# Performance work log

Measured on AMD Instinct MI355X. Metric: run time of the kernel, lower is better.

Reference implementation:

```python
import jax, jax.numpy as jnp
import numpy as np

N = 100000      # nodes (== hyperedges, H is square: adjacency-derived incidence)
NNZ = 3200000   # nonzeros in H
IN, HID, OUT = 512, 16, 64


def setup_inputs() -> dict:
    key = jax.random.key(0)
    ks = jax.random.split(key, 8)
    row = jax.random.randint(ks[0], (NNZ,), 0, N)
    col = jax.random.randint(ks[1], (NNZ,), 0, N)
    values = jnp.ones((NNZ,), dtype=jnp.float32)
    X = jax.random.normal(ks[2], (N, IN), dtype=jnp.float32)
    W1 = jax.random.normal(ks[3], (HID, IN), dtype=jnp.float32) * 0.05
    b1 = jax.random.normal(ks[4], (HID,), dtype=jnp.float32) * 0.05
    W2 = jax.random.normal(ks[5], (OUT, HID), dtype=jnp.float32) * 0.05
    b2 = jax.random.normal(ks[6], (OUT,), dtype=jnp.float32) * 0.05
    return {"row": row, "col": col, "values": values, "X": X,
            "W1": W1, "b1": b1, "W2": W2, "b2": b2}


def reference(row, col, values, X, W1, b1, W2, b2):
    # Degrees: d_V = H.sum(1) over rows, d_E = H.sum(0) over cols
    d_V = jax.ops.segment_sum(values, row, num_segments=N)
    d_E = jax.ops.segment_sum(values, col, num_segments=N)
    dv = d_V ** -0.5          # D_V^-1/2 diagonal
    de = d_E ** -1.0          # D_E^-1 diagonal (W = I, folded in)

    def conv(Y):
        # D_V^-1/2 @ H @ D_E^-1 @ H^T @ D_V^-1/2 @ Y, via edge-list SpMMs
        Y1 = Y * dv[:, None]
        # Z = H^T @ Y1 : scatter v * Y1[row] into hyperedge bins (col)
        Z = jax.ops.segment_sum(values[:, None] * Y1[row], col, num_segments=N)
        Z = Z * de[:, None]
        # O = H @ Z : scatter v * Z[col] back into node bins (row)
        O = jax.ops.segment_sum(values[:, None] * Z[col], row, num_segments=N)
        return O * dv[:, None]

    # dropout is identity in eval mode
    H1 = jax.nn.relu(conv(X @ W1.T + b1))      # [N, HID]
    out = conv(H1 @ W2.T + b2)                  # [N, OUT]
    return out
```

## Files before the change

### kernel.cpp

```cpp
#include <hip/hip_runtime.h>

#define NN 100000
#define NNZ 3200000
#define DIN 512
#define DHID 16
#define DOUT 64
#define NBUK 391
#define BCAP 9216
#define EPB 4096
#define NBLK_A ((NNZ + EPB - 1) / EPB)

#define GLOBAL_AS __attribute__((address_space(1)))
#define LDS_AS    __attribute__((address_space(3)))


__global__ __launch_bounds__(256) void init_cur_kernel(
    int* __restrict__ cur_c, int* __restrict__ cur_r) {
    int i = blockIdx.x * 256 + threadIdx.x;
    if (i < NBUK) { cur_c[i] = i * BCAP; cur_r[i] = i * BCAP; }
}

__global__ __launch_bounds__(256) void bucket_scatter_kernel(
    const int* __restrict__ row, const int* __restrict__ col,
    int* __restrict__ cur_c, int* __restrict__ cur_r,
    int* __restrict__ stgc, int* __restrict__ stgr) {
    __shared__ int stage[EPB];
    __shared__ unsigned short binOf[EPB];
    __shared__ int hist[512], scn[256], lof[512], curb[512], gdelta[512];
    int side = blockIdx.y;
    const int* key = side ? row : col;
    const int* oth = side ? col : row;
    int* gcur = side ? cur_r : cur_c;
    int* gstg = side ? stgr : stgc;
    int tid = threadIdx.x;
    int m = NNZ - blockIdx.x * EPB; if (m > EPB) m = EPB;
    int e0 = blockIdx.x * EPB + tid;

    hist[tid] = 0; hist[tid + 256] = 0;
    __syncthreads();
    #pragma unroll 4
    for (int u = 0; u < EPB / 256; ++u) {
        if (tid + u * 256 < m) atomicAdd(&hist[key[e0 + u * 256] >> 8], 1);
    }
    __syncthreads();
    int s0 = hist[2 * tid], s1 = hist[2 * tid + 1];
    int ps = s0 + s1;
    scn[tid] = ps;
    __syncthreads();
    for (int d = 1; d < 256; d <<= 1) {
        int t = (tid >= d) ? scn[tid - d] : 0;
        __syncthreads();
        scn[tid] += t;
        __syncthreads();
    }
    int excl = scn[tid] - ps;
    lof[2 * tid] = excl;
    lof[2 * tid + 1] = excl + s0;
    curb[2 * tid] = excl;
    curb[2 * tid + 1] = excl + s0;
    if (2 * tid < NBUK)
        gdelta[2 * tid] = (s0 ? atomicAdd(&gcur[2 * tid], s0) : (2 * tid) * BCAP) - excl;
    if (2 * tid + 1 < NBUK)
        gdelta[2 * tid + 1] = (s1 ? atomicAdd(&gcur[2 * tid + 1], s1) : (2 * tid + 1) * BCAP) - (excl + s0);
    __syncthreads();
    #pragma unroll 2
    for (int u = 0; u < EPB / 256; ++u) {
        if (tid + u * 256 < m) {
            int e = e0 + u * 256;
            int k = key[e], o2 = oth[e];
            int bin = k >> 8;
            int pos = atomicAdd(&curb[bin], 1);
            stage[pos] = ((k & 255) << 17) | o2;
            binOf[pos] = (unsigned short)bin;
        }
    }
    __syncthreads();
    for (int i = tid; i < m; i += 256) {
        int bin = binOf[i];
        int dst = gdelta[bin] + i;
        if (dst < (bin + 1) * BCAP) gstg[dst] = stage[i];
    }
}

__global__ __launch_bounds__(256) void bucket_finalize_kernel(
    const int* __restrict__ cur_c, const int* __restrict__ cur_r,
    const int* __restrict__ stgc, const int* __restrict__ stgr,
    int* __restrict__ adjc, int* __restrict__ adjr,
    int* __restrict__ os_c, int* __restrict__ oe_c,
    int* __restrict__ os_r, int* __restrict__ oe_r,
    float* __restrict__ dee, float* __restrict__ dvv) {
    int side = blockIdx.y;
    const int* curv = side ? cur_r : cur_c;
    const int* stg = side ? stgr : stgc;
    int* adj = side ? adjr : adjc;
    int* os = side ? os_r : os_c;
    int* oe = side ? oe_r : oe_c;
    __shared__ int E[BCAP];
    __shared__ int hist[256], cur[256], scn[256];
    int b = blockIdx.x, tid = threadIdx.x;
    int base = b * BCAP;
    int m = curv[b] - base;
    if (m > BCAP) m = BCAP;
    hist[tid] = 0;
    __syncthreads();
    for (int i = tid; i < m; i += 256) {
        int ev = stg[base + i];
        E[i] = ev;
        atomicAdd(&hist[ev >> 17], 1);
    }
    __syncthreads();
    int x = hist[tid];
    scn[tid] = x;
    __syncthreads();
    for (int d = 1; d < 256; d <<= 1) {
        int t = (tid >= d) ? scn[tid - d] : 0;
        __syncthreads();
        scn[tid] += t;
        __syncthreads();
    }
    int excl = scn[tid] - x;
    cur[tid] = excl;
    __syncthreads();
    for (int i = tid; i < m; i += 256) {
        int ev = E[i];
        int nl = ev >> 17;
        int pos = atomicAdd(&cur[nl], 1);
        adj[base + pos] = ev & 0x1FFFF;
    }
    int n = (b << 8) + tid;
    if (n < NN) {
        os[n] = base + excl;
        oe[n] = base + excl + x;
        float xf = (float)x;
        if (side == 0) dee[n] = x > 0 ? 1.0f / xf : 0.f;
        else           dvv[n] = x > 0 ? rsqrtf(xf) : 0.f;
    }
}

__global__ __launch_bounds__(256) void gemm1_kernel(
    const float* __restrict__ X, const float* __restrict__ W1,
    const float* __restrict__ b1, const float* __restrict__ dvv,
    float* __restrict__ Yv) {
    __shared__ float W1s[16 * 516];
    __shared__ float Xs0[16 * 260];
    __shared__ float Xs1[16 * 260];
    int tid = threadIdx.x;
    for (int it = 0; it < 8; ++it) {
        int idx = (it * 256 + tid) << 2;
        int h = idx >> 9, k = idx & 511;
        __builtin_amdgcn_global_load_lds(
            (const GLOBAL_AS void*)(W1 + idx),
            (LDS_AS void*)(W1s + h * 516 + k), 16, 0, 0);
    }
    int n0 = blockIdx.x << 4;
    for (int it = 0; it < 4; ++it) {
        int idx = (it * 256 + tid) << 2;
        int r = idx >> 8, k = idx & 255;
        __builtin_amdgcn_global_load_lds(
            (const GLOBAL_AS void*)(X + (size_t)(n0 + r) * DIN + k),
            (LDS_AS void*)(Xs0 + r * 260 + k), 16, 0, 0);
    }
    __syncthreads();
    for (int it = 0; it < 4; ++it) {
        int idx = (it * 256 + tid) << 2;
        int r = idx >> 8, k = idx & 255;
        __builtin_amdgcn_global_load_lds(
            (const GLOBAL_AS void*)(X + (size_t)(n0 + r) * DIN + 256 + k),
            (LDS_AS void*)(Xs1 + r * 260 + k), 16, 0, 0);
    }
    int n = tid >> 4, h = tid & 15;
    float4 a4 = make_float4(0.f, 0.f, 0.f, 0.f);
    {
        const float4* xr = reinterpret_cast<const float4*>(Xs0 + n * 260);
        const float4* wr = reinterpret_cast<const float4*>(W1s + h * 516);
        #pragma unroll 8
        for (int k4 = 0; k4 < 64; ++k4) {
            float4 xv = xr[k4], wv = wr[k4];
            a4.x = fmaf(xv.x, wv.x, a4.x);
            a4.y = fmaf(xv.y, wv.y, a4.y);
            a4.z = fmaf(xv.z, wv.z, a4.z);
            a4.w = fmaf(xv.w, wv.w, a4.w);
        }
    }
    __syncthreads();
    {
        const float4* xr = reinterpret_cast<const float4*>(Xs1 + n * 260);
        const float4* wr = reinterpret_cast<const float4*>(W1s + h * 516 + 256);
        #pragma unroll 8
        for (int k4 = 0; k4 < 64; ++k4) {
            float4 xv = xr[k4], wv = wr[k4];
            a4.x = fmaf(xv.x, wv.x, a4.x);
            a4.y = fmaf(xv.y, wv.y, a4.y);
            a4.z = fmaf(xv.z, wv.z, a4.z);
            a4.w = fmaf(xv.w, wv.w, a4.w);
        }
    }
    float acc = (a4.x + a4.y) + (a4.z + a4.w);
    int node = n0 + n;
    Yv[node * DHID + h] = (acc + b1[h]) * dvv[node];
}

template<int MODE, int FUSE1, int FUSEOUT>
__global__ __launch_bounds__(256) void gather16_kernel(
    const int* __restrict__ os, const int* __restrict__ oe,
    const int* __restrict__ adj, const float* __restrict__ src,
    const float* __restrict__ sc, const float* __restrict__ src1,
    const float* __restrict__ sc1, float* __restrict__ dst,
    float* __restrict__ dst1, const float* __restrict__ W2,
    const float* __restrict__ b2, const float* __restrict__ g1,
    float* __restrict__ outp) {
    __shared__ float W2t[16 * 64];
    __shared__ float b2s[64];
    int tid = threadIdx.x;
    if (FUSEOUT) {
        #pragma unroll
        for (int q = 0; q < 4; ++q) {
            int idx = (tid << 2) + q;
            int o = idx >> 4, h = idx & 15;
            W2t[h * 64 + o] = W2[idx];
        }
        if (tid < 64) b2s[tid] = b2[tid];
        __syncthreads();
    }
    int t = blockIdx.x * 256 + tid;
    int n = t >> 4, sub = (t >> 2) & 3, f4 = t & 3;
    const float4* src4 = reinterpret_cast<const float4*>(src);
    float4 a0 = make_float4(0.f, 0.f, 0.f, 0.f);
    float4 a1 = make_float4(0.f, 0.f, 0.f, 0.f);
    float4 a2 = make_float4(0.f, 0.f, 0.f, 0.f);
    float4 a3 = make_float4(0.f, 0.f, 0.f, 0.f);
    float acc1 = 0.f;
    int pe = oe[n];
    int p = os[n] + sub;
    for (; p + 12 < pe; p += 16) {
        int j0 = adj[p], j1 = adj[p + 4], j2 = adj[p + 8], j3 = adj[p + 12];
        float4 s0 = src4[(j0 << 2) | f4];
        float4 s1 = src4[(j1 << 2) | f4];
        float4 s2 = src4[(j2 << 2) | f4];
        float4 s3 = src4[(j3 << 2) | f4];
        a0.x += s0.x; a0.y += s0.y; a0.z += s0.z; a0.w += s0.w;
        a1.x += s1.x; a1.y += s1.y; a1.z += s1.z; a1.w += s1.w;
        a2.x += s2.x; a2.y += s2.y; a2.z += s2.z; a2.w += s2.w;
        a3.x += s3.x; a3.y += s3.y; a3.z += s3.z; a3.w += s3.w;
        if (FUSE1 && f4 == 0) acc1 += (src1[j0] + src1[j1]) + (src1[j2] + src1[j3]);
    }
    for (; p < pe; p += 4) {
        int j0 = adj[p];
        float4 s0 = src4[(j0 << 2) | f4];
        a0.x += s0.x; a0.y += s0.y; a0.z += s0.z; a0.w += s0.w;
        if (FUSE1 && f4 == 0) acc1 += src1[j0];
    }
    float4 acc;
    acc.x = (a0.x + a1.x) + (a2.x + a3.x);
    acc.y = (a0.y + a1.y) + (a2.y + a3.y);
    acc.z = (a0.z + a1.z) + (a2.z + a3.z);
    acc.w = (a0.w + a1.w) + (a2.w + a3.w);
    acc.x += __shfl_xor(acc.x, 4); acc.y += __shfl_xor(acc.y, 4);
    acc.z += __shfl_xor(acc.z, 4); acc.w += __shfl_xor(acc.w, 4);
    acc.x += __shfl_xor(acc.x, 8); acc.y += __shfl_xor(acc.y, 8);
    acc.z += __shfl_xor(acc.z, 8); acc.w += __shfl_xor(acc.w, 8);
    if (FUSE1 && f4 == 0) {
        acc1 += __shfl_xor(acc1, 4);
        acc1 += __shfl_xor(acc1, 8);
    }
    if (FUSEOUT) {
        float s = sc[n];
        float T[16];
        #pragma unroll
        for (int q = 0; q < 4; ++q) {
            T[4 * q + 0] = s * __shfl(acc.x, q, 16);
            T[4 * q + 1] = s * __shfl(acc.y, q, 16);
            T[4 * q + 2] = s * __shfl(acc.z, q, 16);
            T[4 * q + 3] = s * __shfl(acc.w, q, 16);
        }
        int l = tid & 15;
        float gn = g1[n];
        float4 o4 = make_float4(0.f, 0.f, 0.f, 0.f);
        #pragma unroll
        for (int h = 0; h < DHID; ++h) {
            float4 w = *reinterpret_cast<const float4*>(&W2t[h * 64 + 4 * l]);
            o4.x = fmaf(T[h], w.x, o4.x);
            o4.y = fmaf(T[h], w.y, o4.y);
            o4.z = fmaf(T[h], w.z, o4.z);
            o4.w = fmaf(T[h], w.w, o4.w);
        }
        float4 bb = *reinterpret_cast<const float4*>(&b2s[4 * l]);
        o4.x = fmaf(gn, bb.x, o4.x);
        o4.y = fmaf(gn, bb.y, o4.y);
        o4.z = fmaf(gn, bb.z, o4.z);
        o4.w = fmaf(gn, bb.w, o4.w);
        reinterpret_cast<float4*>(outp)[(n << 4) | l] = o4;
    } else if (sub == 0) {
        float s = sc[n];
        if (MODE == 1) {
            acc.x *= s; acc.y *= s; acc.z *= s; acc.w *= s;
        } else {
            acc.x = s * fmaxf(s * acc.x, 0.f);
            acc.y = s * fmaxf(s * acc.y, 0.f);
            acc.z = s * fmaxf(s * acc.z, 0.f);
            acc.w = s * fmaxf(s * acc.w, 0.f);
        }
        reinterpret_cast<float4*>(dst)[(n << 2) | f4] = acc;
        if (FUSE1 && f4 == 0) dst1[n] = acc1 * sc1[n];
    }
}

extern "C" void kernel_launch(void* const* d_in, const int* in_sizes, int n_in,
                              void* d_out, int out_size, void* d_ws, size_t ws_size,
                              hipStream_t stream) {
    const int*   row    = (const int*)d_in[0];
    const int*   col    = (const int*)d_in[1];
    const float* X      = (const float*)d_in[3];
    const float* W1     = (const float*)d_in[4];
    const float* b1     = (const float*)d_in[5];
    const float* W2     = (const float*)d_in[6];
    const float* b2     = (const float*)d_in[7];
    float* out = (float*)d_out;

    char* ws = (char*)d_ws;
    size_t o = 0;
    auto alloc = [&](size_t elems) {
        void* p = ws + o; o += (elems * 4 + 15) & ~size_t(15); return p;
    };

    int*   cur_c = (int*)alloc(NBUK);
    int*   cur_r = (int*)alloc(NBUK);
    int*   os_c  = (int*)alloc(NN);
    int*   oe_c  = (int*)alloc(NN);
    int*   os_r  = (int*)alloc(NN);
    int*   oe_r  = (int*)alloc(NN);
    float* dvv   = (float*)alloc(NN);
    float* dee   = (float*)alloc(NN);
    float* ue    = (float*)alloc(NN);
    float* gv    = (float*)alloc(NN);
    int*   stgc  = (int*)alloc((size_t)NBUK * BCAP);
    int*   stgr  = (int*)alloc((size_t)NBUK * BCAP);
    int*   adjc  = (int*)alloc((size_t)NBUK * BCAP);
    int*   adjr  = (int*)alloc((size_t)NBUK * BCAP);
    float* Yv    = (float*)alloc((size_t)NN * DHID);
    float* Z1    = (float*)alloc((size_t)NN * DHID);
    float* Sv    = (float*)alloc((size_t)NN * DHID);
    float* Z2    = (float*)alloc((size_t)NN * DHID);

    init_cur_kernel<<<dim3((NBUK + 255) / 256), dim3(256), 0, stream>>>(cur_c, cur_r);
    bucket_scatter_kernel<<<dim3(NBLK_A, 2), dim3(256), 0, stream>>>(
        row, col, cur_c, cur_r, stgc, stgr);
    bucket_finalize_kernel<<<dim3(NBUK, 2), dim3(256), 0, stream>>>(
        cur_c, cur_r, stgc, stgr, adjc, adjr, os_c, oe_c, os_r, oe_r, dee, dvv);

    gemm1_kernel<<<dim3(NN / 16), dim3(256), 0, stream>>>(X, W1, b1, dvv, Yv);

    int gblk = NN * 16 / 256;
    gather16_kernel<1, 1, 0><<<dim3(gblk), dim3(256), 0, stream>>>(
        os_c, oe_c, adjc, Yv, dee, dvv, dee, Z1, ue,
        nullptr, nullptr, nullptr, nullptr);
    gather16_kernel<2, 1, 0><<<dim3(gblk), dim3(256), 0, stream>>>(
        os_r, oe_r, adjr, Z1, dvv, ue, dvv, Sv, gv,
        nullptr, nullptr, nullptr, nullptr);

    gather16_kernel<1, 0, 0><<<dim3(gblk), dim3(256), 0, stream>>>(
        os_c, oe_c, adjc, Sv, dee, nullptr, nullptr, Z2, nullptr,
        nullptr, nullptr, nullptr, nullptr);
    gather16_kernel<1, 0, 1><<<dim3(gblk), dim3(256), 0, stream>>>(
        os_r, oe_r, adjr, Z2, dvv, nullptr, nullptr, nullptr, nullptr,
        W2, b2, gv, out);
}
```

Before: 363.5 us.

## Vectorize bucket loads, use wave-shuffle scans, async-stage finalize input, single-buffer gemm1

The bucket scatter kernel now reads keys and partner indices as int4 vectors, and both bucketing kernels replace the LDS Hillis-Steele block scan with a wavefront shuffle scan plus per-wave totals. The finalize kernel copies its staged bucket into LDS with global_load_lds before building the histogram. gemm1 goes from two X staging buffers to one reused buffer loaded per 256-column chunk. This cuts barriers and load instructions and lowers LDS use in gemm1, but it removes the overlap between loading the second X half and computing the first.

```diff
diff --git a/kernel.cpp b/kernel.cpp
--- a/kernel.cpp
+++ b/kernel.cpp
@@ -26,7 +26,8 @@
     int* __restrict__ stgc, int* __restrict__ stgr) {
     __shared__ int stage[EPB];
     __shared__ unsigned short binOf[EPB];
-    __shared__ int hist[512], scn[256], lof[512], curb[512], gdelta[512];
+    __shared__ int hist[512], lof[512], curb[512], gdelta[512];
+    __shared__ int wtot[4];
     int side = blockIdx.y;
     const int* key = side ? row : col;
     const int* oth = side ? col : row;
@@ -34,26 +35,39 @@
     int* gstg = side ? stgr : stgc;
     int tid = threadIdx.x;
     int m = NNZ - blockIdx.x * EPB; if (m > EPB) m = EPB;
-    int e0 = blockIdx.x * EPB + tid;
+    int m4 = m >> 2;
+    const int4* key4 = reinterpret_cast<const int4*>(key + blockIdx.x * EPB);
+    const int4* oth4 = reinterpret_cast<const int4*>(oth + blockIdx.x * EPB);
 
     hist[tid] = 0; hist[tid + 256] = 0;
     __syncthreads();
-    #pragma unroll 4
-    for (int u = 0; u < EPB / 256; ++u) {
-        if (tid + u * 256 < m) atomicAdd(&hist[key[e0 + u * 256] >> 8], 1);
+    #pragma unroll
+    for (int u = 0; u < EPB / 1024; ++u) {
+        int i4 = u * 256 + tid;
+        if (i4 < m4) {
+            int4 k = key4[i4];
+            atomicAdd(&hist[k.x >> 8], 1);
+            atomicAdd(&hist[k.y >> 8], 1);
+            atomicAdd(&hist[k.z >> 8], 1);
+            atomicAdd(&hist[k.w >> 8], 1);
+        }
     }
     __syncthreads();
     int s0 = hist[2 * tid], s1 = hist[2 * tid + 1];
     int ps = s0 + s1;
-    scn[tid] = ps;
-    __syncthreads();
-    for (int d = 1; d < 256; d <<= 1) {
-        int t = (tid >= d) ? scn[tid - d] : 0;
-        __syncthreads();
-        scn[tid] += t;
-        __syncthreads();
-    }
-    int excl = scn[tid] - ps;
+    int lane = tid & 63, wid = tid >> 6;
+    int v = ps;
+    #pragma unroll
+    for (int d = 1; d < 64; d <<= 1) {
+        int t2 = __shfl_up(v, d);
+        if (lane >= d) v += t2;
+    }
+    if (lane == 63) wtot[wid] = v;
+    __syncthreads();
+    int wbase = 0;
+    #pragma unroll
+    for (int w = 0; w < 3; ++w) wbase += (w < wid) ? wtot[w] : 0;
+    int excl = (v + wbase) - ps;
     lof[2 * tid] = excl;
     lof[2 * tid + 1] = excl + s0;
     curb[2 * tid] = excl;
@@ -63,15 +77,20 @@
     if (2 * tid + 1 < NBUK)
         gdelta[2 * tid + 1] = (s1 ? atomicAdd(&gcur[2 * tid + 1], s1) : (2 * tid + 1) * BCAP) - (excl + s0);
     __syncthreads();
-    #pragma unroll 2
-    for (int u = 0; u < EPB / 256; ++u) {
-        if (tid + u * 256 < m) {
-            int e = e0 + u * 256;
-            int k = key[e], o2 = oth[e];
-            int bin = k >> 8;
-            int pos = atomicAdd(&curb[bin], 1);
-            stage[pos] = ((k & 255) << 17) | o2;
-            binOf[pos] = (unsigned short)bin;
+    #pragma unroll
+    for (int u = 0; u < EPB / 1024; ++u) {
+        int i4 = u * 256 + tid;
+        if (i4 < m4) {
+            int4 k = key4[i4], o = oth4[i4];
+            int bin, pos;
+            bin = k.x >> 8; pos = atomicAdd(&curb[bin], 1);
+            stage[pos] = ((k.x & 255) << 17) | o.x; binOf[pos] = (unsigned short)bin;
+            bin = k.y >> 8; pos = atomicAdd(&curb[bin], 1);
+            stage[pos] = ((k.y & 255) << 17) | o.y; binOf[pos] = (unsigned short)bin;
+            bin = k.z >> 8; pos = atomicAdd(&curb[bin], 1);
+            stage[pos] = ((k.z & 255) << 17) | o.z; binOf[pos] = (unsigned short)bin;
+            bin = k.w >> 8; pos = atomicAdd(&curb[bin], 1);
+            stage[pos] = ((k.w & 255) << 17) | o.w; binOf[pos] = (unsigned short)bin;
         }
     }
     __syncthreads();
@@ -96,29 +115,38 @@
     int* os = side ? os_r : os_c;
     int* oe = side ? oe_r : oe_c;
     __shared__ int E[BCAP];
-    __shared__ int hist[256], cur[256], scn[256];
+    __shared__ int hist[256], cur[256];
+    __shared__ int wtot[4];
     int b = blockIdx.x, tid = threadIdx.x;
     int base = b * BCAP;
     int m = curv[b] - base;
     if (m > BCAP) m = BCAP;
     hist[tid] = 0;
+    int nIter = (m + 1023) >> 10;
+    for (int k = 0; k < nIter; ++k) {
+        __builtin_amdgcn_global_load_lds(
+            (const GLOBAL_AS void*)(stg + base + k * 1024 + tid * 4),
+            (LDS_AS void*)(E + k * 1024 + tid * 4), 16, 0, 0);
+    }
     __syncthreads();
     for (int i = tid; i < m; i += 256) {
-        int ev = stg[base + i];
-        E[i] = ev;
-        atomicAdd(&hist[ev >> 17], 1);
+        atomicAdd(&hist[E[i] >> 17], 1);
     }
     __syncthreads();
     int x = hist[tid];
-    scn[tid] = x;
-    __syncthreads();
-    for (int d = 1; d < 256; d <<= 1) {
-        int t = (tid >= d) ? scn[tid - d] : 0;
-        __syncthreads();
-        scn[tid] += t;
-        __syncthreads();
-    }
-    int excl = scn[tid] - x;
+    int lane = tid & 63, wid = tid >> 6;
+    int v = x;
+    #pragma unroll
+    for (int d = 1; d < 64; d <<= 1) {
+        int t2 = __shfl_up(v, d);
+        if (lane >= d) v += t2;
+    }
+    if (lane == 63) wtot[wid] = v;
+    __syncthreads();
+    int wbase = 0;
+    #pragma unroll
+    for (int w = 0; w < 3; ++w) wbase += (w < wid) ? wtot[w] : 0;
+    int excl = (v + wbase) - x;
     cur[tid] = excl;
     __syncthreads();
     for (int i = tid; i < m; i += 256) {
@@ -142,8 +170,7 @@
     const float* __restrict__ b1, const float* __restrict__ dvv,
     float* __restrict__ Yv) {
     __shared__ float W1s[16 * 516];
-    __shared__ float Xs0[16 * 260];
-    __shared__ float Xs1[16 * 260];
+    __shared__ float Xs[16 * 260];
     int tid = threadIdx.x;
     for (int it = 0; it < 8; ++it) {
         int idx = (it * 256 + tid) << 2;
@@ -153,39 +180,20 @@
             (LDS_AS void*)(W1s + h * 516 + k), 16, 0, 0);
     }
     int n0 = blockIdx.x << 4;
-    for (int it = 0; it < 4; ++it) {
-        int idx = (it * 256 + tid) << 2;
-        int r = idx >> 8, k = idx & 255;
-        __builtin_amdgcn_global_load_lds(
-            (const GLOBAL_AS void*)(X + (size_t)(n0 + r) * DIN + k),
-            (LDS_AS void*)(Xs0 + r * 260 + k), 16, 0, 0);
-    }
-    __syncthreads();
-    for (int it = 0; it < 4; ++it) {
-        int idx = (it * 256 + tid) << 2;
-        int r = idx >> 8, k = idx & 255;
-        __builtin_amdgcn_global_load_lds(
-            (const GLOBAL_AS void*)(X + (size_t)(n0 + r) * DIN + 256 + k),
-            (LDS_AS void*)(Xs1 + r * 260 + k), 16, 0, 0);
-    }
     int n = tid >> 4, h = tid & 15;
     float4 a4 = make_float4(0.f, 0.f, 0.f, 0.f);
-    {
-        const float4* xr = reinterpret_cast<const float4*>(Xs0 + n * 260);
-        const float4* wr = reinterpret_cast<const float4*>(W1s + h * 516);
-        #pragma unroll 8
-        for (int k4 = 0; k4 < 64; ++k4) {
-            float4 xv = xr[k4], wv = wr[k4];
-            a4.x = fmaf(xv.x, wv.x, a4.x);
-            a4.y = fmaf(xv.y, wv.y, a4.y);
-            a4.z = fmaf(xv.z, wv.z, a4.z);
-            a4.w = fmaf(xv.w, wv.w, a4.w);
-        }
-    }
-    __syncthreads();
-    {
-        const float4* xr = reinterpret_cast<const float4*>(Xs1 + n * 260);
-        const float4* wr = reinterpret_cast<const float4*>(W1s + h * 516 + 256);
+    for (int ck = 0; ck < 512; ck += 256) {
+        __syncthreads();
+        for (int it = 0; it < 4; ++it) {
+            int idx = (it * 256 + tid) << 2;
+            int r = idx >> 8, k = idx & 255;
+            __builtin_amdgcn_global_load_lds(
+                (const GLOBAL_AS void*)(X + (size_t)(n0 + r) * DIN + ck + k),
+                (LDS_AS void*)(Xs + r * 260 + k), 16, 0, 0);
+        }
+        __syncthreads();
+        const float4* xr = reinterpret_cast<const float4*>(Xs + n * 260);
+        const float4* wr = reinterpret_cast<const float4*>(W1s + h * 516 + ck);
         #pragma unroll 8
         for (int k4 = 0; k4 < 64; ++k4) {
             float4 xv = xr[k4], wv = wr[k4];
```

Result: faster. 333.7 us (-8.2%).
